# Kernel optimization log

Measured on AMD Instinct MI355X. Metric: run time of the kernel, lower is better.

## Reference

```python
import jax, jax.numpy as jnp
import numpy as np

K = 3
STRIDE = 1
PAD = 1


def conv2d(x, w, b):
    # standard NCHW conv, stride 1, pad 1
    out = jax.lax.conv_general_dilated(
        x, w, (STRIDE, STRIDE), [(PAD, PAD), (PAD, PAD)],
        dimension_numbers=("NCHW", "OIHW", "NCHW"))
    return out + b[None, :, None, None]


def deform_conv2d(x, offset, mask, weight):
    # torchvision.ops.deform_conv2d semantics (offset_groups=1):
    # offset: [B, 2*K*K, Ho, Wo] laid out as (k, (y, x)) per kernel tap k (row-major)
    # mask:   [B, K*K, Ho, Wo]
    B, C, H, W = x.shape
    KK = K * K
    Ho, Wo = offset.shape[2:]
    off = offset.reshape(B, KK, 2, Ho, Wo)

    # base sampling positions: p = out*stride - pad + kernel_tap + offset
    tap_y = jnp.repeat(jnp.arange(K, dtype=x.dtype), K)  # [KK]
    tap_x = jnp.tile(jnp.arange(K, dtype=x.dtype), K)    # [KK]
    grid_y = jnp.arange(Ho, dtype=x.dtype) * STRIDE - PAD
    grid_x = jnp.arange(Wo, dtype=x.dtype) * STRIDE - PAD
    py = grid_y[None, None, :, None] + tap_y[None, :, None, None] + off[:, :, 0]  # [B,KK,Ho,Wo]
    px = grid_x[None, None, None, :] + tap_x[None, :, None, None] + off[:, :, 1]

    y0 = jnp.floor(py)
    x0 = jnp.floor(px)
    wy1 = py - y0  # fractional parts
    wx1 = px - x0

    xf = x.reshape(B, C, H * W)

    def gather(yi, xi):
        # zero-padding semantics: out-of-bounds corners contribute 0
        valid = (yi >= 0) & (yi <= H - 1) & (xi >= 0) & (xi <= W - 1)
        idx = (jnp.clip(yi, 0, H - 1) * W + jnp.clip(xi, 0, W - 1)).astype(jnp.int32)
        v = jnp.take_along_axis(xf, idx.reshape(B, 1, KK * Ho * Wo), axis=2)
        v = v.reshape(B, C, KK, Ho, Wo)
        return v * valid[:, None].astype(x.dtype)

    e = lambda a: a[:, None]  # [B,KK,Ho,Wo] -> [B,1,KK,Ho,Wo]
    sampled = (gather(y0, x0) * e((1 - wy1) * (1 - wx1))
               + gather(y0, x0 + 1) * e((1 - wy1) * wx1)
               + gather(y0 + 1, x0) * e(wy1 * (1 - wx1))
               + gather(y0 + 1, x0 + 1) * e(wy1 * wx1))
    sampled = sampled * mask[:, None]  # modulated, [B,C,KK,Ho,Wo]

    Cout = weight.shape[0]
    out = jnp.einsum("bckhw,ock->bohw", sampled, weight.reshape(Cout, C, KK))
    return out


def setup_inputs() -> dict:
    key = jax.random.key(0)
    ks = jax.random.split(key, 5)
    B, Cin, Cout, H, W = 4, 128, 256, 64, 64
    x = jax.random.normal(ks[0], (B, Cin, H, W), jnp.float32)
    # offset/modulator convs are zero-init in the module; use small random weights
    # so the deformable sampling path is actually exercised
    offset_w = jax.random.normal(ks[1], (2 * K * K, Cin, K, K), jnp.float32) * 0.02
    offset_b = jax.random.normal(ks[2], (2 * K * K,), jnp.float32) * 0.1
    mod_w = jax.random.normal(ks[3], (K * K, Cin, K, K), jnp.float32) * 0.02
    mod_b = jnp.zeros((K * K,), jnp.float32)
    weight = jax.random.normal(ks[4], (Cout, Cin, K, K), jnp.float32) * (1.0 / np.sqrt(Cin * K * K))
    return {"x": x, "offset_w": offset_w, "offset_b": offset_b,
            "mod_w": mod_w, "mod_b": mod_b, "weight": weight}


def reference(x, offset_w, offset_b, mod_w, mod_b, weight):
    H, W = x.shape[2], x.shape[3]
    max_offset = max(H, W) / 4.0
    offset = jnp.clip(conv2d(x, offset_w, offset_b), -max_offset, max_offset)
    mask = 2.0 * jax.nn.sigmoid(conv2d(x, mod_w, mod_b))
    return deform_conv2d(x, offset, mask, weight)
```

## Files before the change

kernel.cpp:

```cpp
#include <hip/hip_runtime.h>
#include <math.h>

#define CIN   128
#define COUT  256
#define HH    64
#define WW    64
#define BB    4
#define KK    9
#define CK    (CIN*KK)

typedef unsigned short u16;
typedef unsigned int   u32;
using f32x4  = __attribute__((ext_vector_type(4))) float;
using s16x8  = __attribute__((ext_vector_type(8))) short;

__device__ __forceinline__ u16 f2bf(float f) {
    union { float f; u32 u; } v; v.f = f;
    u32 u = v.u;
    u += 0x7FFFu + ((u >> 16) & 1u);
    return (u16)(u >> 16);
}
__device__ __forceinline__ float bfel(s16x8 v, int j) {
    union { u32 u; float f; } c; c.u = ((u32)(u16)v[j]) << 16; return c.f;
}
__device__ __forceinline__ u32 asu(float f) {
    union { float f; u32 u; } v; v.f = f; return v.u;
}

__global__ __launch_bounds__(256)
void prep_all(const float* __restrict__ x, const float* __restrict__ w,
              const float* __restrict__ ow, const float* __restrict__ mw,
              u16* __restrict__ xt, u16* __restrict__ wfrag,
              u16* __restrict__ wofsf) {
    __shared__ u16 T[64][130];
    int blk = blockIdx.x;
    int tid = threadIdx.x;

    if (blk < 256) {
        int b = blk >> 6, y = blk & 63;
        int lane = tid & 63, cw = tid >> 6;
        for (int c = cw; c < 128; c += 4)
            T[lane][c] = f2bf(x[((b * 128 + c) * 64 + y) * 64 + lane]);
        __syncthreads();
        int c = tid & 127;
        for (int p = tid >> 7; p < 64; p += 2)
            xt[((b * 64 + y) * 64 + p) * 128 + c] = T[p][c];
    } else if (blk < 256 + 1152) {
        int i = (blk - 256) * 256 + tid;
        int j    = i & 7;
        int lane = (i >> 3) & 63;
        int ks4  = (i >> 9) & 3;
        int t    = (i >> 11) & 1;
        int wv   = (i >> 12) & 7;
        int tap  = i >> 15;
        int co = (wv * 2 + t) * 16 + (lane & 15);
        int k  = tap * 128 + ks4 * 32 + (lane >> 4) * 8 + j;
        int c  = k & 127;
        wfrag[i] = f2bf(w[co * CK + c * 9 + tap]);
    } else {
        int i = (blk - 1408) * 256 + tid;
        if (i < 9 * 4096) {
            int j    = i & 7;
            int lane = (i >> 3) & 63;
            int ks4  = (i >> 9) & 3;
            int t    = (i >> 11) & 1;
            int tap  = i >> 12;
            int co = t * 16 + (lane & 15);
            int k  = tap * 128 + ks4 * 32 + (lane >> 4) * 8 + j;
            int c  = k & 127;
            float v = 0.f;
            if (co < 18)      v = ow[co * CK + c * 9 + tap];
            else if (co < 27) v = mw[(co - 18) * CK + c * 9 + tap];
            wofsf[i] = f2bf(v);
        }
    }
}

__global__ __launch_bounds__(512, 4)
void dcn_fused(const u16* __restrict__ xt, const u16* __restrict__ wofsf,
               const float* __restrict__ ob, const float* __restrict__ mb,
               const u16* __restrict__ wfrag, float* __restrict__ out) {
    int blkid = blockIdx.x;
    int xcd = blkid & 7, idx = blkid >> 3;
    int b   = xcd >> 1;
    int ho  = ((xcd & 1) << 5) + (idx >> 1);
    int wo0 = (idx & 1) << 5;
    int tid = threadIdx.x;

    __shared__ __align__(16) u16 Sm[4][32][136];
    __shared__ float s_om[27][32];
    __shared__ int   s_idx[32][KK][4];
    __shared__ float s_wgt[32][KK][4];

    int wv   = tid >> 6, lane = tid & 63;
    int quad = lane >> 4, l16 = lane & 15;
    int gpx  = wv * 4 + (lane >> 4);
    int oct  = lane & 15;

    const u16* xtb = xt + (size_t)b * 4096 * 128;
    const s16x8 vzero = {0,0,0,0,0,0,0,0};

    int pa_ph = wv & 1;
    f32x4 aco[2];
    aco[0] = (f32x4)(0.f); aco[1] = (f32x4)(0.f);

    s16x8 sA[2][2];
    auto pa_gather = [&](int tap, int sp, int ti) {
        int kx = tap % 3;
        int y  = ho - 1 + tap / 3;
        bool yok = (unsigned)y < HH;
        int col = wo0 + gpx + kx - 1;
        bool ok = yok && ((unsigned)col < WW);
        int yc = yok ? y : 0;
        int cc = ((unsigned)col < WW) ? col : 0;
        s16x8 v = *(const s16x8*)(xtb + (size_t)(yc * 64 + cc) * 128 + oct * 8);
        sA[sp][ti] = ok ? v : vzero;
    };

    auto pa_mfma_tap = [&](int tap, int slot) {
        const u16* wc = wofsf + tap * 4096 + lane * 8;
#pragma unroll
        for (int ks4 = 0; ks4 < 4; ++ks4) {
            s16x8 bfrag = *(const s16x8*)(&Sm[slot][pa_ph * 16 + l16][ks4 * 32 + quad * 8]);
#pragma unroll
            for (int t = 0; t < 2; ++t) {
                s16x8 afrag = *(const s16x8*)(wc + (t * 4 + ks4) * 512);
                aco[t] = __builtin_amdgcn_mfma_f32_16x16x32_bf16(afrag, bfrag, aco[t], 0, 0, 0);
            }
        }
    };

    pa_gather(0, 0, 0);
    pa_gather(1, 0, 1);
#pragma unroll
    for (int p = 0; p < 4; ++p) {
        int sp = p & 1;
        *(s16x8*)(&Sm[2 * sp    ][gpx][oct * 8]) = sA[sp][0];
        *(s16x8*)(&Sm[2 * sp + 1][gpx][oct * 8]) = sA[sp][1];
        __syncthreads();
        if (p < 3) { pa_gather(2 * p + 2, sp ^ 1, 0); pa_gather(2 * p + 3, sp ^ 1, 1); }
        else       { pa_gather(8,         sp ^ 1, 0); }
        if (wv < 2) {
            pa_mfma_tap(2 * p,     2 * sp);
            pa_mfma_tap(2 * p + 1, 2 * sp + 1);
        }
    }
    *(s16x8*)(&Sm[0][gpx][oct * 8]) = sA[0][0];
    __syncthreads();
    if (wv < 2) pa_mfma_tap(8, 0);

    if (wv < 2) {
#pragma unroll
        for (int t = 0; t < 2; ++t) {
#pragma unroll
            for (int r = 0; r < 4; ++r) {
                int co = t * 16 + quad * 4 + r;
                if (co < 27) {
                    float v = aco[t][r];
                    if (co < 18) {
                        v += ob[co];
                        v = fminf(fmaxf(v, -16.f), 16.f);
                    } else {
                        v += mb[co - 18];
                        v = 2.f / (1.f + expf(-v));
                    }
                    s_om[co][pa_ph * 16 + l16] = v;
                }
            }
        }
    }
    __syncthreads();

    if (tid < 32 * KK) {
        int p = tid / KK, k = tid - (tid / KK) * KK;
        int wo = wo0 + p;
        float offy = s_om[2 * k][p];
        float offx = s_om[2 * k + 1][p];
        float mval = s_om[18 + k][p];

        float py = (float)(ho - 1 + k / 3) + offy;
        float px = (float)(wo - 1 + k % 3) + offx;
        float y0f = floorf(py), x0f = floorf(px);
        float wy1 = py - y0f,  wx1 = px - x0f;
        float wy0 = 1.f - wy1, wx0 = 1.f - wx1;
        int iy0 = (int)y0f, ix0 = (int)x0f;
        int iy1 = iy0 + 1,  ix1 = ix0 + 1;
        bool vy0 = (iy0 >= 0) && (iy0 < HH);
        bool vy1 = (iy1 >= 0) && (iy1 < HH);
        bool vx0 = (ix0 >= 0) && (ix0 < WW);
        bool vx1 = (ix1 >= 0) && (ix1 < WW);
        int cy0 = min(max(iy0, 0), HH - 1), cy1 = min(max(iy1, 0), HH - 1);
        int cx0 = min(max(ix0, 0), WW - 1), cx1 = min(max(ix1, 0), WW - 1);
        s_idx[p][k][0] = (cy0 * WW + cx0) * 128;
        s_idx[p][k][1] = (cy0 * WW + cx1) * 128;
        s_idx[p][k][2] = (cy1 * WW + cx0) * 128;
        s_idx[p][k][3] = (cy1 * WW + cx1) * 128;
        s_wgt[p][k][0] = (vy0 && vx0) ? mval * wy0 * wx0 : 0.f;
        s_wgt[p][k][1] = (vy0 && vx1) ? mval * wy0 * wx1 : 0.f;
        s_wgt[p][k][2] = (vy1 && vx0) ? mval * wy1 * wx0 : 0.f;
        s_wgt[p][k][3] = (vy1 && vx1) ? mval * wy1 * wx1 : 0.f;
    }
    __syncthreads();

    f32x4 acc[2][2];
#pragma unroll
    for (int t = 0; t < 2; ++t) { acc[t][0] = (f32x4)(0.f); acc[t][1] = (f32x4)(0.f); }

    s16x8 crs[2][2][4];
    float gs[2][2][4];
    auto gatherB = [&](int tap, int sp, int ti) {
        int i0 = s_idx[gpx][tap][0], i1 = s_idx[gpx][tap][1];
        int i2 = s_idx[gpx][tap][2], i3 = s_idx[gpx][tap][3];
        gs[sp][ti][0] = s_wgt[gpx][tap][0]; gs[sp][ti][1] = s_wgt[gpx][tap][1];
        gs[sp][ti][2] = s_wgt[gpx][tap][2]; gs[sp][ti][3] = s_wgt[gpx][tap][3];
        int co8 = oct * 8;
        crs[sp][ti][0] = *(const s16x8*)(xtb + i0 + co8);
        crs[sp][ti][1] = *(const s16x8*)(xtb + i1 + co8);
        crs[sp][ti][2] = *(const s16x8*)(xtb + i2 + co8);
        crs[sp][ti][3] = *(const s16x8*)(xtb + i3 + co8);
    };

    auto blend_store = [&](int sp, int ti, int slot) {
        float g0 = gs[sp][ti][0], g1 = gs[sp][ti][1];
        float g2 = gs[sp][ti][2], g3 = gs[sp][ti][3];
        float o[8];
#pragma unroll
        for (int j = 0; j < 8; ++j)
            o[j] = g0 * bfel(crs[sp][ti][0], j) + g1 * bfel(crs[sp][ti][1], j)
                 + g2 * bfel(crs[sp][ti][2], j) + g3 * bfel(crs[sp][ti][3], j);
        uint4 pkv;
        pkv.x = (asu(o[1]) & 0xFFFF0000u) | (asu(o[0]) >> 16);
        pkv.y = (asu(o[3]) & 0xFFFF0000u) | (asu(o[2]) >> 16);
        pkv.z = (asu(o[5]) & 0xFFFF0000u) | (asu(o[4]) >> 16);
        pkv.w = (asu(o[7]) & 0xFFFF0000u) | (asu(o[6]) >> 16);
        *(uint4*)(&Sm[slot][gpx][oct * 8]) = pkv;
    };

    auto pb_mfma_tap = [&](int tap, int slot) {
        const u16* wc = wfrag + (tap * 8 + wv) * 4096 + lane * 8;
        s16x8 af[8];
#pragma unroll
        for (int t = 0; t < 2; ++t)
#pragma unroll
            for (int ks4 = 0; ks4 < 4; ++ks4)
                af[t * 4 + ks4] = *(const s16x8*)(wc + (t * 4 + ks4) * 512);
#pragma unroll
        for (int ks4 = 0; ks4 < 4; ++ks4) {
            s16x8 bf0 = *(const s16x8*)(&Sm[slot][l16][ks4 * 32 + quad * 8]);
            s16x8 bf1 = *(const s16x8*)(&Sm[slot][16 + l16][ks4 * 32 + quad * 8]);
#pragma unroll
            for (int t = 0; t < 2; ++t) {
                acc[t][0] = __builtin_amdgcn_mfma_f32_16x16x32_bf16(af[t * 4 + ks4], bf0, acc[t][0], 0, 0, 0);
                acc[t][1] = __builtin_amdgcn_mfma_f32_16x16x32_bf16(af[t * 4 + ks4], bf1, acc[t][1], 0, 0, 0);
            }
        }
    };

    gatherB(0, 0, 0);
    gatherB(1, 0, 1);
#pragma unroll
    for (int p = 0; p < 4; ++p) {
        int sp = p & 1;
        blend_store(sp, 0, 2 * sp);
        blend_store(sp, 1, 2 * sp + 1);
        __syncthreads();
        if (p < 3) { gatherB(2 * p + 2, sp ^ 1, 0); gatherB(2 * p + 3, sp ^ 1, 1); }
        else       { gatherB(8,         sp ^ 1, 0); }
        pb_mfma_tap(2 * p,     2 * sp);
        pb_mfma_tap(2 * p + 1, 2 * sp + 1);
    }
    blend_store(0, 0, 0);
    __syncthreads();
    pb_mfma_tap(8, 0);

#pragma unroll
    for (int t = 0; t < 2; ++t) {
        int cobase = (wv * 2 + t) * 16 + quad * 4;
#pragma unroll
        for (int ph = 0; ph < 2; ++ph) {
#pragma unroll
            for (int r = 0; r < 4; ++r) {
                int co = cobase + r;
                out[((b * COUT + co) * HH + ho) * WW + wo0 + ph * 16 + l16] = acc[t][ph][r];
            }
        }
    }
}

extern "C" void kernel_launch(void* const* d_in, const int* in_sizes, int n_in,
                              void* d_out, int out_size, void* d_ws, size_t ws_size,
                              hipStream_t stream) {
    const float* x  = (const float*)d_in[0];
    const float* ow = (const float*)d_in[1];
    const float* ob = (const float*)d_in[2];
    const float* mw = (const float*)d_in[3];
    const float* mb = (const float*)d_in[4];
    const float* wt = (const float*)d_in[5];

    char* ws = (char*)d_ws;
    u16* wfrag = (u16*)ws;  ws += (size_t)COUT * CK * 2;
    u16* wofsf = (u16*)ws;  ws += (size_t)32 * CK * 2;
    u16* xt    = (u16*)ws;
    float* out = (float*)d_out;

    prep_all<<<1552, 256, 0, stream>>>(x, wt, ow, mw, xt, wfrag, wofsf);

    dcn_fused<<<BB * HH * 2, 512, 0, stream>>>(xt, wofsf, ob, mb, wfrag, out);
}
```

Baseline: 103.6 us.

## Compute offset/mask conv with direct register gathers instead of LDS staging

The offset/modulator conv phase no longer stages input tiles through shared memory with per-tap __syncthreads. Four waves now each own one (output-channel-tile, pixel-half) combination and load their MFMA B fragments straight from global memory into registers, double-buffered across taps. This removes the barriers and LDS round-trips from the first phase and puts four waves to work instead of two, at the cost of redundant global loads across waves and more registers. An unused variable is also added in the second phase.

Result: no change. 104.6 us (+1.0%).

```diff
diff --git a/kernel.cpp b/kernel.cpp
--- a/kernel.cpp
+++ b/kernel.cpp
@@ -100,72 +100,54 @@
     const u16* xtb = xt + (size_t)b * 4096 * 128;
     const s16x8 vzero = {0,0,0,0,0,0,0,0};
 
-    int pa_ph = wv & 1;
-    f32x4 aco[2];
-    aco[0] = (f32x4)(0.f); aco[1] = (f32x4)(0.f);
-
-    s16x8 sA[2][2];
-    auto pa_gather = [&](int tap, int sp, int ti) {
-        int kx = tap % 3;
-        int y  = ho - 1 + tap / 3;
-        bool yok = (unsigned)y < HH;
-        int col = wo0 + gpx + kx - 1;
-        bool ok = yok && ((unsigned)col < WW);
-        int yc = yok ? y : 0;
-        int cc = ((unsigned)col < WW) ? col : 0;
-        s16x8 v = *(const s16x8*)(xtb + (size_t)(yc * 64 + cc) * 128 + oct * 8);
-        sA[sp][ti] = ok ? v : vzero;
-    };
-
-    auto pa_mfma_tap = [&](int tap, int slot) {
-        const u16* wc = wofsf + tap * 4096 + lane * 8;
-#pragma unroll
-        for (int ks4 = 0; ks4 < 4; ++ks4) {
-            s16x8 bfrag = *(const s16x8*)(&Sm[slot][pa_ph * 16 + l16][ks4 * 32 + quad * 8]);
-#pragma unroll
-            for (int t = 0; t < 2; ++t) {
-                s16x8 afrag = *(const s16x8*)(wc + (t * 4 + ks4) * 512);
-                aco[t] = __builtin_amdgcn_mfma_f32_16x16x32_bf16(afrag, bfrag, aco[t], 0, 0, 0);
-            }
-        }
-    };
-
-    pa_gather(0, 0, 0);
-    pa_gather(1, 0, 1);
-#pragma unroll
-    for (int p = 0; p < 4; ++p) {
-        int sp = p & 1;
-        *(s16x8*)(&Sm[2 * sp    ][gpx][oct * 8]) = sA[sp][0];
-        *(s16x8*)(&Sm[2 * sp + 1][gpx][oct * 8]) = sA[sp][1];
-        __syncthreads();
-        if (p < 3) { pa_gather(2 * p + 2, sp ^ 1, 0); pa_gather(2 * p + 3, sp ^ 1, 1); }
-        else       { pa_gather(8,         sp ^ 1, 0); }
-        if (wv < 2) {
-            pa_mfma_tap(2 * p,     2 * sp);
-            pa_mfma_tap(2 * p + 1, 2 * sp + 1);
-        }
-    }
-    *(s16x8*)(&Sm[0][gpx][oct * 8]) = sA[0][0];
-    __syncthreads();
-    if (wv < 2) pa_mfma_tap(8, 0);
-
-    if (wv < 2) {
-#pragma unroll
-        for (int t = 0; t < 2; ++t) {
-#pragma unroll
-            for (int r = 0; r < 4; ++r) {
-                int co = t * 16 + quad * 4 + r;
-                if (co < 27) {
-                    float v = aco[t][r];
-                    if (co < 18) {
-                        v += ob[co];
-                        v = fminf(fmaxf(v, -16.f), 16.f);
-                    } else {
-                        v += mb[co - 18];
-                        v = 2.f / (1.f + expf(-v));
-                    }
-                    s_om[co][pa_ph * 16 + l16] = v;
+    if (wv < 4) {
+        int t  = wv >> 1;
+        int ph = wv & 1;
+        int wo = wo0 + ph * 16 + l16;
+        f32x4 aco = (f32x4)(0.f);
+
+        s16x8 bA[2][4];
+        auto loadB = [&](int tap, int slot) {
+            int kx = tap % 3;
+            int y  = ho - 1 + tap / 3;
+            int col = wo + kx - 1;
+            bool ok = ((unsigned)y < HH) && ((unsigned)col < WW);
+            int yc = ok ? y : 0, cc = ok ? col : 0;
+            const u16* base = xtb + (size_t)(yc * 64 + cc) * 128 + quad * 8;
+#pragma unroll
+            for (int ks4 = 0; ks4 < 4; ++ks4) {
+                s16x8 v = *(const s16x8*)(base + ks4 * 32);
+                bA[slot][ks4] = ok ? v : vzero;
+            }
+        };
+
+        loadB(0, 0);
+        loadB(1, 1);
+#pragma unroll
+        for (int tap = 0; tap < 9; ++tap) {
+            int sl = tap & 1;
+            const u16* wc = wofsf + (tap * 2 + t) * 2048 + lane * 8;
+#pragma unroll
+            for (int ks4 = 0; ks4 < 4; ++ks4) {
+                s16x8 afrag = *(const s16x8*)(wc + ks4 * 512);
+                aco = __builtin_amdgcn_mfma_f32_16x16x32_bf16(afrag, bA[sl][ks4], aco, 0, 0, 0);
+            }
+            if (tap + 2 < 9) loadB(tap + 2, sl);
+        }
+
+#pragma unroll
+        for (int r = 0; r < 4; ++r) {
+            int co = t * 16 + quad * 4 + r;
+            if (co < 27) {
+                float v = aco[r];
+                if (co < 18) {
+                    v += ob[co];
+                    v = fminf(fmaxf(v, -16.f), 16.f);
+                } else {
+                    v += mb[co - 18];
+                    v = 2.f / (1.f + expf(-v));
                 }
+                s_om[co][ph * 16 + l16] = v;
             }
         }
     }
@@ -258,6 +240,7 @@
 
     gatherB(0, 0, 0);
     gatherB(1, 0, 1);
+    int buf = 0;
 #pragma unroll
     for (int p = 0; p < 4; ++p) {
         int sp = p & 1;
```
